# Optimization experiments

Hardware: AMD Instinct MI355X
Metric: run time of the kernel (lower is better)

## Reference

```python
import jax, jax.numpy as jnp
import numpy as np

N = 20000      # nodes
E = 320000     # edges (before self-loops)
DIN = 128      # input_dim
HID = 256      # hidden_dim
HEADS = 8
C = HID // HEADS  # per-head channels = 32
G = 16         # graphs in batch
OUT = 2
EPS = 1e-5


def setup_inputs() -> dict:
    key = jax.random.key(0)
    ks = jax.random.split(key, 24)

    def lin(k, fan_in, fan_out):
        return jax.random.normal(k, (fan_in, fan_out), jnp.float32) / np.float32(np.sqrt(fan_in))

    inp = {
        "x": jax.random.normal(ks[0], (N, DIN), jnp.float32),
        "edge_index": jax.random.randint(ks[1], (2, E), 0, N, jnp.int64),
        "batch": jnp.sort(jax.random.randint(ks[2], (N,), 0, G, jnp.int64)),
        # encoder
        "enc_w": lin(ks[3], DIN, HID), "enc_b": jnp.zeros((HID,), jnp.float32),
        # gat1 (GATv2: lin_l, lin_r, att, out bias)
        "g1_wl": lin(ks[4], HID, HID), "g1_bl": jnp.zeros((HID,), jnp.float32),
        "g1_wr": lin(ks[5], HID, HID), "g1_br": jnp.zeros((HID,), jnp.float32),
        "g1_att": jax.random.normal(ks[6], (HEADS, C), jnp.float32) / np.float32(np.sqrt(C)),
        "g1_bias": jnp.zeros((HID,), jnp.float32),
        # gat2
        "g2_wl": lin(ks[7], HID, HID), "g2_bl": jnp.zeros((HID,), jnp.float32),
        "g2_wr": lin(ks[8], HID, HID), "g2_br": jnp.zeros((HID,), jnp.float32),
        "g2_att": jax.random.normal(ks[9], (HEADS, C), jnp.float32) / np.float32(np.sqrt(C)),
        "g2_bias": jnp.zeros((HID,), jnp.float32),
        # layernorm
        "ln_g": jnp.ones((HID,), jnp.float32), "ln_b": jnp.zeros((HID,), jnp.float32),
        # head MLP
        "h1_w": lin(ks[10], HID, HID // 2), "h1_b": jnp.zeros((HID // 2,), jnp.float32),
        "h2_w": lin(ks[11], HID // 2, OUT), "h2_b": jnp.zeros((OUT,), jnp.float32),
    }
    return inp


def _gatv2(x, src, dst, wl, bl, wr, br, att, bias, n):
    # GATv2Conv (PyG semantics, eval mode so dropout is identity)
    h, c = att.shape
    xl = (x @ wl + bl).reshape(n, h, c)   # source transform
    xr = (x @ wr + br).reshape(n, h, c)   # target transform
    e = jax.nn.leaky_relu(xl[src] + xr[dst], 0.2)       # [E, H, C]
    score = jnp.einsum('ehc,hc->eh', e, att)            # [E, H]
    smax = jax.ops.segment_max(score, dst, num_segments=n)
    ex = jnp.exp(score - smax[dst])
    denom = jax.ops.segment_sum(ex, dst, num_segments=n)
    alpha = ex / denom[dst]                             # segment softmax over incoming edges
    out = jax.ops.segment_sum(alpha[:, :, None] * xl[src], dst, num_segments=n)
    return out.reshape(n, h * c) + bias


def _layernorm(x, g, b):
    mu = jnp.mean(x, axis=-1, keepdims=True)
    var = jnp.mean(jnp.square(x - mu), axis=-1, keepdims=True)
    return (x - mu) * jax.lax.rsqrt(var + EPS) * g + b


def reference(x, edge_index, batch, enc_w, enc_b,
              g1_wl, g1_bl, g1_wr, g1_br, g1_att, g1_bias,
              g2_wl, g2_bl, g2_wr, g2_br, g2_att, g2_bias,
              ln_g, ln_b, h1_w, h1_b, h2_w, h2_b):
    n = x.shape[0]
    # PyG GATv2Conv default add_self_loops=True
    loops = jnp.arange(n, dtype=edge_index.dtype)
    src = jnp.concatenate([edge_index[0], loops])
    dst = jnp.concatenate([edge_index[1], loops])

    h = jax.nn.relu(x @ enc_w + enc_b)
    h = jax.nn.relu(_gatv2(h, src, dst, g1_wl, g1_bl, g1_wr, g1_br, g1_att, g1_bias, n))
    h = _layernorm(h, ln_g, ln_b)
    h = jax.nn.relu(_gatv2(h, src, dst, g2_wl, g2_bl, g2_wr, g2_br, g2_att, g2_bias, n))

    # global_mean_pool over graph ids
    sums = jax.ops.segment_sum(h, batch, num_segments=G)
    counts = jax.ops.segment_sum(jnp.ones((n,), h.dtype), batch, num_segments=G)
    pooled = sums / jnp.maximum(counts, 1.0)[:, None]

    out = jax.nn.relu(pooled @ h1_w + h1_b) @ h2_w + h2_b
    return out
```

## Files before the change

kernel.cpp:

```cpp
#include <hip/hip_runtime.h>
#include <hip/hip_fp16.h>

#define HIDDIM 256
#define NHEADS 8
#define SCORE_SHIFT 4.0f
#define XSTR 512
#define BPAD 40

struct __attribute__((aligned(8))) half4s { __half2 a, b; };

typedef _Float16 f16x8 __attribute__((ext_vector_type(8)));
typedef float f32x4 __attribute__((ext_vector_type(4)));

__global__ __launch_bounds__(256) void cvt_f2h(
    const float* __restrict__ in, __half* __restrict__ out, int n) {
  const int i = blockIdx.x * 256 + threadIdx.x;
  if (i < n) out[i] = __float2half(in[i]);
}

__global__ __launch_bounds__(256) void cvt_transpose(
    const float* __restrict__ in, __half* __restrict__ out, int K, int N) {
  const int idx = blockIdx.x * 256 + threadIdx.x;
  if (idx >= K * N) return;
  const int n = idx / K, k = idx - n * K;
  out[idx] = __float2half(in[(size_t)k * N + n]);
}

__global__ __launch_bounds__(256) void cvt_transpose4(
    const float* __restrict__ w0, const float* __restrict__ w1,
    const float* __restrict__ w2, const float* __restrict__ w3,
    __half* __restrict__ o0, __half* __restrict__ o1,
    __half* __restrict__ o2, __half* __restrict__ o3) {
  const float* in; __half* out;
  switch (blockIdx.y) {
    case 0: in = w0; out = o0; break;
    case 1: in = w1; out = o1; break;
    case 2: in = w2; out = o2; break;
    default: in = w3; out = o3; break;
  }
  const int idx = blockIdx.x * 256 + threadIdx.x;
  if (idx >= HIDDIM * HIDDIM) return;
  const int n = idx / HIDDIM, k = idx - n * HIDDIM;
  out[idx] = __float2half(in[(size_t)k * HIDDIM + n]);
}

__global__ __launch_bounds__(256) void concat_biases(
    const float* __restrict__ bl0, const float* __restrict__ br0,
    const float* __restrict__ bl1, const float* __restrict__ br1,
    float* __restrict__ o0, float* __restrict__ o1) {
  const int i = blockIdx.x * 256 + threadIdx.x;
  if (i >= 2 * XSTR) return;
  const int layer = i >> 9, pos = i & (XSTR - 1);
  const float* bl = layer ? bl1 : bl0;
  const float* br = layer ? br1 : br0;
  float v = (pos < HIDDIM) ? bl[pos] : br[pos - HIDDIM];
  (layer ? o1 : o0)[pos] = v;
}

template <int RELU, int KT>
__global__ __launch_bounds__(256) void gemm_mfma(
    const _Float16* __restrict__ A, const _Float16* __restrict__ Wt,
    const float* __restrict__ bias, _Float16* __restrict__ C,
    int M, int N) {
  __shared__ _Float16 Bs[128 * BPAD];
  const int tid = threadIdx.x;
  const int wv = tid >> 6;
  const int lane = tid & 63;
  const int bn = blockIdx.x * 128;
  const int bm = blockIdx.y * 128 + wv * 32;
  const int fr = lane & 15;
  const int kb = lane >> 4;

  int ar0 = bm + fr;      if (ar0 >= M) ar0 = M - 1;
  int ar1 = bm + 16 + fr; if (ar1 >= M) ar1 = M - 1;
  const _Float16* ap0 = A + (size_t)ar0 * KT + kb * 8;
  const _Float16* ap1 = A + (size_t)ar1 * KT + kb * 8;

  const int sc = tid >> 2;
  const int sch = (tid & 3) * 8;

  f32x4 acc[2][8] = {};
  #pragma unroll
  for (int k0 = 0; k0 < KT; k0 += 32) {
    const f16x8 a0 = *(const f16x8*)(ap0 + k0);
    const f16x8 a1 = *(const f16x8*)(ap1 + k0);
    const f16x8 s0 = *(const f16x8*)(Wt + (size_t)(bn + sc) * KT + k0 + sch);
    const f16x8 s1 = *(const f16x8*)(Wt + (size_t)(bn + 64 + sc) * KT + k0 + sch);
    __syncthreads();
    *(f16x8*)(Bs + sc * BPAD + sch) = s0;
    *(f16x8*)(Bs + (64 + sc) * BPAD + sch) = s1;
    __syncthreads();
    #pragma unroll
    for (int nt = 0; nt < 8; ++nt) {
      const f16x8 b = *(const f16x8*)(Bs + (nt * 16 + fr) * BPAD + kb * 8);
      acc[0][nt] = __builtin_amdgcn_mfma_f32_16x16x32_f16(a0, b, acc[0][nt], 0, 0, 0);
      acc[1][nt] = __builtin_amdgcn_mfma_f32_16x16x32_f16(a1, b, acc[1][nt], 0, 0, 0);
    }
  }
  #pragma unroll
  for (int g = 0; g < 2; ++g) {
    #pragma unroll
    for (int r = 0; r < 4; ++r) {
      const int row = bm + g * 16 + (lane >> 4) * 4 + r;
      if (row >= M) continue;
      #pragma unroll
      for (int nt = 0; nt < 8; ++nt) {
        const int col = bn + nt * 16 + fr;
        float v = acc[g][nt][r] + bias[col];
        if (RELU && v < 0.f) v = 0.f;
        C[(size_t)row * N + col] = (_Float16)v;
      }
    }
  }
}

__global__ __launch_bounds__(256) void count_deg(
    const int* __restrict__ ei, int* __restrict__ deg, int E, int Nn) {
  const int t = blockIdx.x * blockDim.x + threadIdx.x;
  const int ET = E + Nn;
  if (t >= ET) return;
  const int dst = (t < E) ? ei[E + t] : (t - E);
  atomicAdd(&deg[dst], 1);
}

__global__ __launch_bounds__(1024) void scan_deg(
    const int* __restrict__ deg, int* __restrict__ rowptr, int Nn) {
  const int tid = threadIdx.x;
  const int wid = tid >> 6, lane = tid & 63;
  const int CH = (Nn + 1023) >> 10;
  const int base = tid * CH;
  int s[32];
  int run = 0;
  #pragma unroll
  for (int i = 0; i < 32; ++i) {
    if (i < CH) {
      const int idx = base + i;
      const int v = (idx < Nn) ? deg[idx] : 0;
      run += v;
    }
    s[i] = run;
  }
  int tot = run;
  #pragma unroll
  for (int off = 1; off < 64; off <<= 1) {
    int t = __shfl_up(tot, off);
    if (lane >= off) tot += t;
  }
  __shared__ int wsum[16];
  __shared__ int wpre[16];
  if (lane == 63) wsum[wid] = tot;
  __syncthreads();
  if (tid < 16) {
    int ws = wsum[tid];
    #pragma unroll
    for (int off = 1; off < 16; off <<= 1) {
      int t = __shfl_up(ws, off);
      if (tid >= off) ws += t;
    }
    wpre[tid] = ws;
  }
  __syncthreads();
  const int excl = (wid ? wpre[wid - 1] : 0) + (tot - run);
  #pragma unroll
  for (int i = 0; i < 32; ++i) {
    if (i < CH) {
      const int idx = base + i;
      if (idx < Nn) rowptr[idx + 1] = excl + s[i];
    }
  }
  if (tid == 0) rowptr[0] = 0;
}

__global__ __launch_bounds__(256) void fill_csr(
    const int* __restrict__ ei, const int* __restrict__ rowptr,
    int* __restrict__ cursor, int* __restrict__ csr, int E, int Nn) {
  const int t = blockIdx.x * blockDim.x + threadIdx.x;
  const int ET = E + Nn;
  if (t >= ET) return;
  int src, dst;
  if (t < E) { src = ei[t]; dst = ei[E + t]; }
  else { src = t - E; dst = t - E; }
  const int pos = atomicAdd(&cursor[dst], 1);
  csr[rowptr[dst] + pos] = src;
}

__global__ __launch_bounds__(256) void graph_ranges(
    const int* __restrict__ batch, int* __restrict__ gstart, int Nn, int G) {
  const int n = blockIdx.x * 256 + threadIdx.x;
  if (n > Nn) return;
  if (n == 0) {
    for (int g = 0; g <= batch[0]; ++g) gstart[g] = 0;
  } else if (n == Nn) {
    for (int g = batch[Nn - 1] + 1; g <= G; ++g) gstart[g] = Nn;
  } else {
    const int b = batch[n], bp = batch[n - 1];
    for (int g = bp + 1; g <= b; ++g) gstart[g] = n;
  }
}

template <int MODE>
__global__ __launch_bounds__(256) void node_gat(
    const __half* __restrict__ xlr,
    const int* __restrict__ rowptr, const int* __restrict__ csr,
    const float* __restrict__ att, const float* __restrict__ bias,
    const float* __restrict__ lng, const float* __restrict__ lnb,
    __half* __restrict__ outp, int Nn) {
  int n = (int)((blockIdx.x * (size_t)blockDim.x + threadIdx.x) >> 6);
  const int lane = threadIdx.x & 63;
  if (n >= Nn) return;
  n = __builtin_amdgcn_readfirstlane(n);
  const int r0 = rowptr[n], r1 = rowptr[n + 1];
  const int jm = r1 - 1;
  const half4s* __restrict__ xlv = (const half4s*)xlr;
  float4 xr4;
  {
    const half4s xrh = xlv[(size_t)n * (XSTR / 4) + 64 + lane];
    const float2 f01 = __half22float2(xrh.a);
    const float2 f23 = __half22float2(xrh.b);
    xr4 = make_float4(f01.x, f01.y, f23.x, f23.y);
  }
  const float4 at4 = *(const float4*)(att + lane * 4);
  float4 acc = make_float4(0.f, 0.f, 0.f, 0.f);
  float den = 0.f;

  for (int j0 = r0; j0 <= jm; j0 += 8) {
    half4s r[8];
    #pragma unroll
    for (int k = 0; k < 8; ++k) {
      int j = j0 + k; j = j <= jm ? j : jm;
      r[k] = xlv[(size_t)csr[j] * (XSTR / 4) + lane];
    }
    float4 a[8];
    float s[8];
    #pragma unroll
    for (int k = 0; k < 8; ++k) {
      const float2 f01 = __half22float2(r[k].a);
      const float2 f23 = __half22float2(r[k].b);
      a[k] = make_float4(f01.x, f01.y, f23.x, f23.y);
      float v, ss;
      v = a[k].x + xr4.x; v = v >= 0.f ? v : 0.2f * v; ss = v * at4.x;
      v = a[k].y + xr4.y; v = v >= 0.f ? v : 0.2f * v; ss = fmaf(v, at4.y, ss);
      v = a[k].z + xr4.z; v = v >= 0.f ? v : 0.2f * v; ss = fmaf(v, at4.z, ss);
      v = a[k].w + xr4.w; v = v >= 0.f ? v : 0.2f * v; ss = fmaf(v, at4.w, ss);
      s[k] = ss;
    }
    #pragma unroll
    for (int k = 0; k < 8; ++k) {
      s[k] += __shfl_xor(s[k], 1);
      s[k] += __shfl_xor(s[k], 2);
      s[k] += __shfl_xor(s[k], 4);
    }
    float w[8];
    #pragma unroll
    for (int k = 0; k < 8; ++k)
      w[k] = (j0 + k <= jm) ? __expf(s[k] - SCORE_SHIFT) : 0.f;
    #pragma unroll
    for (int k = 0; k < 8; ++k) {
      acc.x = fmaf(w[k], a[k].x, acc.x);
      acc.y = fmaf(w[k], a[k].y, acc.y);
      acc.z = fmaf(w[k], a[k].z, acc.z);
      acc.w = fmaf(w[k], a[k].w, acc.w);
      den += w[k];
    }
  }
  const float inv_d = 1.f / den;
  const float4 bb = *(const float4*)(bias + lane * 4);
  float t0 = fmaf(acc.x, inv_d, bb.x); t0 = t0 > 0.f ? t0 : 0.f;
  float t1 = fmaf(acc.y, inv_d, bb.y); t1 = t1 > 0.f ? t1 : 0.f;
  float t2 = fmaf(acc.z, inv_d, bb.z); t2 = t2 > 0.f ? t2 : 0.f;
  float t3 = fmaf(acc.w, inv_d, bb.w); t3 = t3 > 0.f ? t3 : 0.f;

  if (MODE == 0) {
    float s = t0 + t1 + t2 + t3;
    #pragma unroll
    for (int mm = 1; mm < 64; mm <<= 1) s += __shfl_xor(s, mm);
    const float mu = s * (1.f / HIDDIM);
    const float d0 = t0 - mu, d1 = t1 - mu, d2 = t2 - mu, d3 = t3 - mu;
    float q = d0 * d0 + d1 * d1 + d2 * d2 + d3 * d3;
    #pragma unroll
    for (int mm = 1; mm < 64; mm <<= 1) q += __shfl_xor(q, mm);
    const float inv = rsqrtf(q * (1.f / HIDDIM) + 1e-5f);
    const float4 g4 = *(const float4*)(lng + lane * 4);
    const float4 b4 = *(const float4*)(lnb + lane * 4);
    half4s ho;
    ho.a = __floats2half2_rn(d0 * inv * g4.x + b4.x, d1 * inv * g4.y + b4.y);
    ho.b = __floats2half2_rn(d2 * inv * g4.z + b4.z, d3 * inv * g4.w + b4.w);
    *((half4s*)outp + (size_t)n * (HIDDIM / 4) + lane) = ho;
  } else {
    half4s ho;
    ho.a = __floats2half2_rn(t0, t1);
    ho.b = __floats2half2_rn(t2, t3);
    *((half4s*)outp + (size_t)n * (HIDDIM / 4) + lane) = ho;
  }
}

__global__ __launch_bounds__(256) void pool_kernel(
    const __half* __restrict__ tbuf, const int* __restrict__ gstart,
    float* __restrict__ pooled) {
  const int g = blockIdx.x, rc = blockIdx.y, ch = threadIdx.x;
  const int n0 = gstart[g], n1 = gstart[g + 1];
  float acc = 0.f;
  for (int n = n0 + rc; n < n1; n += 8)
    acc += __half2float(tbuf[(size_t)n * HIDDIM + ch]);
  atomicAdd(&pooled[g * HIDDIM + ch], acc);
}

__global__ __launch_bounds__(256) void head_kernel(
    const float* __restrict__ pooled, const int* __restrict__ gstart,
    const float* __restrict__ h1w, const float* __restrict__ h1b,
    const float* __restrict__ h2w, const float* __restrict__ h2b,
    float* __restrict__ out, int H1, int OUT) {
  const int g = blockIdx.x;
  __shared__ float P[HIDDIM];
  __shared__ float Hh[128];
  const int tid = threadIdx.x;
  float cnt = (float)(gstart[g + 1] - gstart[g]);
  if (cnt < 1.f) cnt = 1.f;
  P[tid] = pooled[g * HIDDIM + tid] / cnt;
  __syncthreads();
  if (tid < H1) {
    float s = h1b[tid];
    for (int k = 0; k < HIDDIM; ++k) s = fmaf(P[k], h1w[k * H1 + tid], s);
    Hh[tid] = s > 0.f ? s : 0.f;
  }
  __syncthreads();
  if (tid < OUT) {
    float s = h2b[tid];
    for (int k = 0; k < H1; ++k) s = fmaf(Hh[k], h2w[k * OUT + tid], s);
    out[g * OUT + tid] = s;
  }
}

extern "C" void kernel_launch(void* const* d_in, const int* in_sizes, int n_in,
                              void* d_out, int out_size, void* d_ws, size_t ws_size,
                              hipStream_t stream) {
  const float* x = (const float*)d_in[0];
  const int* ei = (const int*)d_in[1];
  const int* batch = (const int*)d_in[2];
  const float* enc_w = (const float*)d_in[3];
  const float* enc_b = (const float*)d_in[4];
  const float* g_wl[2] = {(const float*)d_in[5], (const float*)d_in[11]};
  const float* g_bl[2] = {(const float*)d_in[6], (const float*)d_in[12]};
  const float* g_wr[2] = {(const float*)d_in[7], (const float*)d_in[13]};
  const float* g_br[2] = {(const float*)d_in[8], (const float*)d_in[14]};
  const float* g_att[2] = {(const float*)d_in[9], (const float*)d_in[15]};
  const float* g_bias[2] = {(const float*)d_in[10], (const float*)d_in[16]};
  const float* ln_g = (const float*)d_in[17];
  const float* ln_b = (const float*)d_in[18];
  const float* h1_w = (const float*)d_in[19];
  const float* h1_b = (const float*)d_in[20];
  const float* h2_w = (const float*)d_in[21];
  const float* h2_b = (const float*)d_in[22];
  float* out = (float*)d_out;

  const int N = in_sizes[2];
  const int E = in_sizes[1] / 2;
  const int DIN = in_sizes[0] / N;
  const int ET = E + N;
  const int H1 = in_sizes[20];
  const int OUT = in_sizes[22];
  const int G = out_size / OUT;

  char* base = (char*)d_ws;
  const size_t NH = (size_t)N * HIDDIM;
  __half* h16  = (__half*)base;
  __half* xlr  = h16 + NH;
  __half* tbuf = xlr + NH * 2;
  __half* x16  = tbuf + NH;
  __half* wtE  = x16 + (size_t)N * DIN;
  __half* wtC0 = wtE + (size_t)HIDDIM * DIN;
  __half* wtC1 = wtC0 + (size_t)XSTR * HIDDIM;
  float* biasC0 = (float*)(wtC1 + (size_t)XSTR * HIDDIM);
  float* biasC1 = biasC0 + XSTR;
  float* pooled = biasC1 + XSTR;
  int* gstart = (int*)(pooled + (size_t)G * HIDDIM);
  int* deg    = gstart + (G + 1);
  int* cursor = deg + N;
  int* rowptr = cursor + N;
  int* csr    = rowptr + (N + 1);

  const dim3 blk(256);
  const int eb = (ET + 255) / 256;
  const int nb = (N + 3) / 4;
  const dim3 enc_grid(HIDDIM / 128, (N + 127) / 128);
  const dim3 cmb_grid(XSTR / 128, (N + 127) / 128);

  hipMemsetAsync(deg, 0, (size_t)2 * N * sizeof(int), stream);
  hipMemsetAsync(pooled, 0, (size_t)G * HIDDIM * sizeof(float), stream);
  count_deg<<<eb, blk, 0, stream>>>(ei, deg, E, N);
  scan_deg<<<1, 1024, 0, stream>>>(deg, rowptr, N);
  fill_csr<<<eb, blk, 0, stream>>>(ei, rowptr, cursor, csr, E, N);
  graph_ranges<<<(N + 256) / 256, blk, 0, stream>>>(batch, gstart, N, G);

  cvt_f2h<<<(N * DIN + 255) / 256, blk, 0, stream>>>(x, x16, N * DIN);
  cvt_transpose<<<(DIN * HIDDIM + 255) / 256, blk, 0, stream>>>(enc_w, wtE, DIN, HIDDIM);
  cvt_transpose4<<<dim3((HIDDIM * HIDDIM + 255) / 256, 4), blk, 0, stream>>>(
      g_wl[0], g_wr[0], g_wl[1], g_wr[1],
      wtC0, wtC0 + (size_t)HIDDIM * HIDDIM, wtC1, wtC1 + (size_t)HIDDIM * HIDDIM);
  concat_biases<<<(2 * XSTR + 255) / 256, blk, 0, stream>>>(
      g_bl[0], g_br[0], g_bl[1], g_br[1], biasC0, biasC1);

  gemm_mfma<1, 128><<<enc_grid, blk, 0, stream>>>(
      (const _Float16*)x16, (const _Float16*)wtE, enc_b, (_Float16*)h16, N, HIDDIM);

  for (int L = 0; L < 2; ++L) {
    const __half* wtC = (L == 0) ? wtC0 : wtC1;
    const float* bC = (L == 0) ? biasC0 : biasC1;
    gemm_mfma<0, 256><<<cmb_grid, blk, 0, stream>>>(
        (const _Float16*)h16, (const _Float16*)wtC, bC, (_Float16*)xlr, N, XSTR);
    if (L == 0) {
      node_gat<0><<<nb, blk, 0, stream>>>(xlr, rowptr, csr, g_att[0], g_bias[0],
                                          ln_g, ln_b, h16, N);
    } else {
      node_gat<1><<<nb, blk, 0, stream>>>(xlr, rowptr, csr, g_att[1], g_bias[1],
                                          nullptr, nullptr, tbuf, N);
      pool_kernel<<<dim3(G, 8), blk, 0, stream>>>(tbuf, gstart, pooled);
    }
  }
  head_kernel<<<G, blk, 0, stream>>>(pooled, gstart, h1_w, h1_b, h2_w, h2_b, out, H1, OUT);
}
```

Before: 245.1 us.

## Fuse fp32-to-fp16 input conversion into encoder GEMM and widen gather batch

The standalone fp32-to-fp16 conversion kernel for x is removed. The encoder GEMM now reads fp32 rows directly and converts them in registers, which saves a kernel launch and one write and read pass over the x buffer. Separately, the per-node GAT aggregation now issues 16 neighbour row gathers per iteration instead of 8, exposing more memory-level parallelism. The cost is more register pressure and occupancy risk in node_gat, plus wider fp32 A loads in the encoder GEMM.

```diff
diff --git a/kernel.cpp b/kernel.cpp
--- a/kernel.cpp
+++ b/kernel.cpp
@@ -11,12 +11,6 @@
 
 typedef _Float16 f16x8 __attribute__((ext_vector_type(8)));
 typedef float f32x4 __attribute__((ext_vector_type(4)));
-
-__global__ __launch_bounds__(256) void cvt_f2h(
-    const float* __restrict__ in, __half* __restrict__ out, int n) {
-  const int i = blockIdx.x * 256 + threadIdx.x;
-  if (i < n) out[i] = __float2half(in[i]);
-}
 
 __global__ __launch_bounds__(256) void cvt_transpose(
     const float* __restrict__ in, __half* __restrict__ out, int K, int N) {
@@ -57,9 +51,23 @@
   (layer ? o1 : o0)[pos] = v;
 }
 
-template <int RELU, int KT>
+__device__ __forceinline__ f16x8 load_a_h(const _Float16* p) {
+  return *(const f16x8*)p;
+}
+__device__ __forceinline__ f16x8 load_a_f(const float* p) {
+  const float4 fa = *(const float4*)p;
+  const float4 fb = *(const float4*)(p + 4);
+  f16x8 r;
+  r[0] = (_Float16)fa.x; r[1] = (_Float16)fa.y;
+  r[2] = (_Float16)fa.z; r[3] = (_Float16)fa.w;
+  r[4] = (_Float16)fb.x; r[5] = (_Float16)fb.y;
+  r[6] = (_Float16)fb.z; r[7] = (_Float16)fb.w;
+  return r;
+}
+
+template <int RELU, int KT, int AF>
 __global__ __launch_bounds__(256) void gemm_mfma(
-    const _Float16* __restrict__ A, const _Float16* __restrict__ Wt,
+    const void* __restrict__ Av, const _Float16* __restrict__ Wt,
     const float* __restrict__ bias, _Float16* __restrict__ C,
     int M, int N) {
   __shared__ _Float16 Bs[128 * BPAD];
@@ -73,8 +81,10 @@
 
   int ar0 = bm + fr;      if (ar0 >= M) ar0 = M - 1;
   int ar1 = bm + 16 + fr; if (ar1 >= M) ar1 = M - 1;
-  const _Float16* ap0 = A + (size_t)ar0 * KT + kb * 8;
-  const _Float16* ap1 = A + (size_t)ar1 * KT + kb * 8;
+  const _Float16* ah0 = (const _Float16*)Av + (size_t)ar0 * KT + kb * 8;
+  const _Float16* ah1 = (const _Float16*)Av + (size_t)ar1 * KT + kb * 8;
+  const float*    af0 = (const float*)Av + (size_t)ar0 * KT + kb * 8;
+  const float*    af1 = (const float*)Av + (size_t)ar1 * KT + kb * 8;
 
   const int sc = tid >> 2;
   const int sch = (tid & 3) * 8;
@@ -82,8 +92,8 @@
   f32x4 acc[2][8] = {};
   #pragma unroll
   for (int k0 = 0; k0 < KT; k0 += 32) {
-    const f16x8 a0 = *(const f16x8*)(ap0 + k0);
-    const f16x8 a1 = *(const f16x8*)(ap1 + k0);
+    const f16x8 a0 = AF ? load_a_f(af0 + k0) : load_a_h(ah0 + k0);
+    const f16x8 a1 = AF ? load_a_f(af1 + k0) : load_a_h(ah1 + k0);
     const f16x8 s0 = *(const f16x8*)(Wt + (size_t)(bn + sc) * KT + k0 + sch);
     const f16x8 s1 = *(const f16x8*)(Wt + (size_t)(bn + 64 + sc) * KT + k0 + sch);
     __syncthreads();
@@ -223,44 +233,48 @@
   float4 acc = make_float4(0.f, 0.f, 0.f, 0.f);
   float den = 0.f;
 
-  for (int j0 = r0; j0 <= jm; j0 += 8) {
-    half4s r[8];
-    #pragma unroll
-    for (int k = 0; k < 8; ++k) {
+  for (int j0 = r0; j0 <= jm; j0 += 16) {
+    half4s r[16];
+    #pragma unroll
+    for (int k = 0; k < 16; ++k) {
       int j = j0 + k; j = j <= jm ? j : jm;
       r[k] = xlv[(size_t)csr[j] * (XSTR / 4) + lane];
     }
-    float4 a[8];
-    float s[8];
-    #pragma unroll
-    for (int k = 0; k < 8; ++k) {
-      const float2 f01 = __half22float2(r[k].a);
-      const float2 f23 = __half22float2(r[k].b);
-      a[k] = make_float4(f01.x, f01.y, f23.x, f23.y);
-      float v, ss;
-      v = a[k].x + xr4.x; v = v >= 0.f ? v : 0.2f * v; ss = v * at4.x;
-      v = a[k].y + xr4.y; v = v >= 0.f ? v : 0.2f * v; ss = fmaf(v, at4.y, ss);
-      v = a[k].z + xr4.z; v = v >= 0.f ? v : 0.2f * v; ss = fmaf(v, at4.z, ss);
-      v = a[k].w + xr4.w; v = v >= 0.f ? v : 0.2f * v; ss = fmaf(v, at4.w, ss);
-      s[k] = ss;
-    }
-    #pragma unroll
-    for (int k = 0; k < 8; ++k) {
-      s[k] += __shfl_xor(s[k], 1);
-      s[k] += __shfl_xor(s[k], 2);
-      s[k] += __shfl_xor(s[k], 4);
-    }
-    float w[8];
-    #pragma unroll
-    for (int k = 0; k < 8; ++k)
-      w[k] = (j0 + k <= jm) ? __expf(s[k] - SCORE_SHIFT) : 0.f;
-    #pragma unroll
-    for (int k = 0; k < 8; ++k) {
-      acc.x = fmaf(w[k], a[k].x, acc.x);
-      acc.y = fmaf(w[k], a[k].y, acc.y);
-      acc.z = fmaf(w[k], a[k].z, acc.z);
-      acc.w = fmaf(w[k], a[k].w, acc.w);
-      den += w[k];
+    #pragma unroll
+    for (int c = 0; c < 2; ++c) {
+      float4 a[8];
+      float s[8];
+      #pragma unroll
+      for (int k = 0; k < 8; ++k) {
+        const int kk = c * 8 + k;
+        const float2 f01 = __half22float2(r[kk].a);
+        const float2 f23 = __half22float2(r[kk].b);
+        a[k] = make_float4(f01.x, f01.y, f23.x, f23.y);
+        float v, ss;
+        v = a[k].x + xr4.x; v = v >= 0.f ? v : 0.2f * v; ss = v * at4.x;
+        v = a[k].y + xr4.y; v = v >= 0.f ? v : 0.2f * v; ss = fmaf(v, at4.y, ss);
+        v = a[k].z + xr4.z; v = v >= 0.f ? v : 0.2f * v; ss = fmaf(v, at4.z, ss);
+        v = a[k].w + xr4.w; v = v >= 0.f ? v : 0.2f * v; ss = fmaf(v, at4.w, ss);
+        s[k] = ss;
+      }
+      #pragma unroll
+      for (int k = 0; k < 8; ++k) {
+        s[k] += __shfl_xor(s[k], 1);
+        s[k] += __shfl_xor(s[k], 2);
+        s[k] += __shfl_xor(s[k], 4);
+      }
+      float w[8];
+      #pragma unroll
+      for (int k = 0; k < 8; ++k)
+        w[k] = (j0 + c * 8 + k <= jm) ? __expf(s[k] - SCORE_SHIFT) : 0.f;
+      #pragma unroll
+      for (int k = 0; k < 8; ++k) {
+        acc.x = fmaf(w[k], a[k].x, acc.x);
+        acc.y = fmaf(w[k], a[k].y, acc.y);
+        acc.z = fmaf(w[k], a[k].z, acc.z);
+        acc.w = fmaf(w[k], a[k].w, acc.w);
+        den += w[k];
+      }
     }
   }
   const float inv_d = 1.f / den;
@@ -366,8 +380,7 @@
   __half* h16  = (__half*)base;
   __half* xlr  = h16 + NH;
   __half* tbuf = xlr + NH * 2;
-  __half* x16  = tbuf + NH;
-  __half* wtE  = x16 + (size_t)N * DIN;
+  __half* wtE  = tbuf + NH;
   __half* wtC0 = wtE + (size_t)HIDDIM * DIN;
   __half* wtC1 = wtC0 + (size_t)XSTR * HIDDIM;
   float* biasC0 = (float*)(wtC1 + (size_t)XSTR * HIDDIM);
@@ -392,7 +405,6 @@
   fill_csr<<<eb, blk, 0, stream>>>(ei, rowptr, cursor, csr, E, N);
   graph_ranges<<<(N + 256) / 256, blk, 0, stream>>>(batch, gstart, N, G);
 
-  cvt_f2h<<<(N * DIN + 255) / 256, blk, 0, stream>>>(x, x16, N * DIN);
   cvt_transpose<<<(DIN * HIDDIM + 255) / 256, blk, 0, stream>>>(enc_w, wtE, DIN, HIDDIM);
   cvt_transpose4<<<dim3((HIDDIM * HIDDIM + 255) / 256, 4), blk, 0, stream>>>(
       g_wl[0], g_wr[0], g_wl[1], g_wr[1],
@@ -400,14 +412,14 @@
   concat_biases<<<(2 * XSTR + 255) / 256, blk, 0, stream>>>(
       g_bl[0], g_br[0], g_bl[1], g_br[1], biasC0, biasC1);
 
-  gemm_mfma<1, 128><<<enc_grid, blk, 0, stream>>>(
-      (const _Float16*)x16, (const _Float16*)wtE, enc_b, (_Float16*)h16, N, HIDDIM);
+  gemm_mfma<1, 128, 1><<<enc_grid, blk, 0, stream>>>(
+      x, (const _Float16*)wtE, enc_b, (_Float16*)h16, N, HIDDIM);
 
   for (int L = 0; L < 2; ++L) {
     const __half* wtC = (L == 0) ? wtC0 : wtC1;
     const float* bC = (L == 0) ? biasC0 : biasC1;
-    gemm_mfma<0, 256><<<cmb_grid, blk, 0, stream>>>(
-        (const _Float16*)h16, (const _Float16*)wtC, bC, (_Float16*)xlr, N, XSTR);
+    gemm_mfma<0, 256, 0><<<cmb_grid, blk, 0, stream>>>(
+        h16, (const _Float16*)wtC, bC, (_Float16*)xlr, N, XSTR);
     if (L == 0) {
       node_gat<0><<<nb, blk, 0, stream>>>(xlr, rowptr, csr, g_att[0], g_bias[0],
                                           ln_g, ln_b, h16, N);
```

Result: no change. 247.1 us (+0.8%).
